# Optimization experiments

Measured on AMD Instinct MI355X. Metric: run time of the kernel, lower is better.

Reference implementation:

```python
import jax, jax.numpy as jnp
import numpy as np

B, C, H, W = 8, 256, 32, 32
N_HEAD = 4
EPS = 1e-5


def setup_inputs() -> dict:
    key = jax.random.key(0)
    ks = jax.random.split(key, 8)
    return {
        "input": jax.random.normal(ks[0], (B, C, H, W), dtype=jnp.float32),
        "bn_gamma": jnp.ones((C,), dtype=jnp.float32),
        "bn_beta": jnp.zeros((C,), dtype=jnp.float32),
        "bn_mean": jax.random.normal(ks[1], (C,), dtype=jnp.float32) * 0.1,
        "bn_var": jax.random.uniform(ks[2], (C,), dtype=jnp.float32, minval=0.5, maxval=1.5),
        "dw_w": jax.random.normal(ks[3], (C,), dtype=jnp.float32) * (1.0 / np.sqrt(C)),
        "pw_w": jax.random.normal(ks[4], (3 * C, C), dtype=jnp.float32) * (1.0 / np.sqrt(C)),
        "out_w": jax.random.normal(ks[5], (C, C), dtype=jnp.float32) * (1.0 / np.sqrt(C)),
        "out_b": jnp.zeros((C,), dtype=jnp.float32),
    }


def reference(input, bn_gamma, bn_beta, bn_mean, bn_var, dw_w, pw_w, out_w, out_b):
    b, c, h, w = input.shape
    n_head = N_HEAD
    head_dim = c // n_head

    # BatchNorm2d (eval mode: running stats), fused with depthwise 1x1 conv
    # (groups=C, kernel 1x1 -> per-channel scalar multiply).
    scale = (bn_gamma * jax.lax.rsqrt(bn_var + EPS) * dw_w)[None, :, None, None]
    shift = (bn_beta * dw_w)[None, :, None, None]
    mean = bn_mean[None, :, None, None]
    x = (input - mean) * scale + shift  # [B,C,H,W]

    # Pointwise 1x1 conv -> QKV: [B, 3C, H, W]
    qkv = jnp.einsum('oc,bchw->bohw', pw_w, x)
    qkv = qkv.reshape(b, n_head, head_dim * 3, h, w)
    q, k, v = jnp.split(qkv, 3, axis=2)  # each [B,n,d,H,W]

    # Full spatial attention logits: [B, n, H, W, H, W]
    attn = jnp.einsum('bnchw,bncyx->bnhwyx', q, k) * (1.0 / np.sqrt(head_dim))
    # Faithful to original: softmax over LAST axis (key x/width) ONLY.
    attn = jax.nn.softmax(attn, axis=-1)

    out = jnp.einsum('bnhwyx,bncyx->bnchw', attn, v).reshape(b, c, h, w)
    out = jnp.einsum('oc,bchw->bohw', out_w, out) + out_b[None, :, None, None]
    return out + input
```

## Files before the change

kernel.cpp:

```cpp
#include <hip/hip_runtime.h>

#define NB 8
#define NC 256
#define NS 1024
#define NHEAD 4
#define HD 64
#define OC 768

#define QSCALE 0.1803368801111204f

typedef float f32x4 __attribute__((ext_vector_type(4)));
typedef __bf16 bf16x8 __attribute__((ext_vector_type(8)));
typedef unsigned short u16;
typedef unsigned int u32;
typedef u16 u16x8 __attribute__((ext_vector_type(8)));
typedef u32 u32x2 __attribute__((ext_vector_type(2)));
typedef int i32x4 __attribute__((ext_vector_type(4)));

__device__ __forceinline__ u16 f2b(float f) {
    return __builtin_bit_cast(u16, (__bf16)f);
}
__device__ __forceinline__ u32 pack2(float lo, float hi) {
    return (u32)f2b(lo) | ((u32)f2b(hi) << 16);
}

__device__ __forceinline__ f32x4 MFMA(u16x8 a, u16x8 b, f32x4 c) {
    return __builtin_amdgcn_mfma_f32_16x16x32_bf16(
        __builtin_bit_cast(bf16x8, a), __builtin_bit_cast(bf16x8, b), c, 0, 0, 0);
}

__global__ void xform(const float* __restrict__ in,
                      const float* __restrict__ gma, const float* __restrict__ bta,
                      const float* __restrict__ mu,  const float* __restrict__ var,
                      const float* __restrict__ dw,  u16* __restrict__ xt) {
    __shared__ float tile[32][33];
    __shared__ float ssc[32], ssh[32];
    int b = blockIdx.z, c0 = blockIdx.y * 32, s0 = blockIdx.x * 32;
    int tx = threadIdx.x & 31, ty = threadIdx.x >> 5;
    if (threadIdx.x < 32) {
        int c = c0 + threadIdx.x;
        float sc = gma[c] * rsqrtf(var[c] + 1e-5f) * dw[c];
        ssc[threadIdx.x] = sc;
        ssh[threadIdx.x] = bta[c] * dw[c] - mu[c] * sc;
    }
    __syncthreads();
#pragma unroll
    for (int r = 0; r < 4; r++) {
        int c = ty + r * 8;
        tile[c][tx] = in[((size_t)b * NC + c0 + c) * NS + s0 + tx] * ssc[c] + ssh[c];
    }
    __syncthreads();
#pragma unroll
    for (int r = 0; r < 4; r++) {
        int s = ty + r * 8;
        xt[((size_t)b * NS + s0 + s) * NC + c0 + tx] = f2b(tile[tx][s]);
    }
}

__global__ __launch_bounds__(256) void qkv_gemm(const float* __restrict__ pw, const u16* __restrict__ xt,
                                                u16* __restrict__ qb, u16* __restrict__ kb,
                                                u16* __restrict__ vb) {
    __shared__ __attribute__((aligned(16))) u16 Ws[64][72];
    __shared__ __attribute__((aligned(16))) u16 Xs[128][72];
    int b = blockIdx.z;
    int m0 = blockIdx.y * 64, n0 = blockIdx.x * 128;
    int tid = threadIdx.x, lane = tid & 63, w = tid >> 6, lg = lane >> 4, li = lane & 15;
    int rowA = tid >> 2, colA = (tid & 3) * 16;
    int rowB = tid >> 1, colB = (tid & 1) * 32;
    const float* pA = pw + (size_t)(m0 + rowA) * NC + colA;
    const u16*   pB = xt + ((size_t)b * NS + n0 + rowB) * NC + colB;
    f32x4 acc[4][2] = {};
#pragma unroll
    for (int k0 = 0; k0 < NC; k0 += 64) {
        __syncthreads();
        f32x4 a0 = *(const f32x4*)(pA + k0);
        f32x4 a1 = *(const f32x4*)(pA + k0 + 4);
        f32x4 a2 = *(const f32x4*)(pA + k0 + 8);
        f32x4 a3 = *(const f32x4*)(pA + k0 + 12);
        i32x4 tb0 = *(const i32x4*)(pB + k0);
        i32x4 tb1 = *(const i32x4*)(pB + k0 + 8);
        i32x4 tb2 = *(const i32x4*)(pB + k0 + 16);
        i32x4 tb3 = *(const i32x4*)(pB + k0 + 24);
        i32x4 wa0, wa1;
        wa0[0] = pack2(a0[0], a0[1]); wa0[1] = pack2(a0[2], a0[3]);
        wa0[2] = pack2(a1[0], a1[1]); wa0[3] = pack2(a1[2], a1[3]);
        wa1[0] = pack2(a2[0], a2[1]); wa1[1] = pack2(a2[2], a2[3]);
        wa1[2] = pack2(a3[0], a3[1]); wa1[3] = pack2(a3[2], a3[3]);
        *(i32x4*)&Ws[rowA][colA]     = wa0;
        *(i32x4*)&Ws[rowA][colA + 8] = wa1;
        *(i32x4*)&Xs[rowB][colB]      = tb0;
        *(i32x4*)&Xs[rowB][colB + 8]  = tb1;
        *(i32x4*)&Xs[rowB][colB + 16] = tb2;
        *(i32x4*)&Xs[rowB][colB + 24] = tb3;
        __syncthreads();
        u16x8 af[4][2], bfr[2][2];
#pragma unroll
        for (int mf = 0; mf < 4; mf++)
#pragma unroll
            for (int kc = 0; kc < 2; kc++)
                af[mf][kc] = *(const u16x8*)&Ws[mf * 16 + li][kc * 32 + lg * 8];
#pragma unroll
        for (int nf = 0; nf < 2; nf++)
#pragma unroll
            for (int kc = 0; kc < 2; kc++)
                bfr[nf][kc] = *(const u16x8*)&Xs[w * 32 + nf * 16 + li][kc * 32 + lg * 8];
#pragma unroll
        for (int kc = 0; kc < 2; kc++)
#pragma unroll
            for (int mf = 0; mf < 4; mf++)
#pragma unroll
                for (int nf = 0; nf < 2; nf++)
                    acc[mf][nf] = MFMA(af[mf][kc], bfr[nf][kc], acc[mf][nf]);
    }
    int sel = (m0 >> 6) % 3;
    int n = m0 / 192;
    size_t bn = (size_t)b * NHEAD + n;
    if (sel == 0) {
#pragma unroll
        for (int mf = 0; mf < 4; mf++)
#pragma unroll
            for (int nf = 0; nf < 2; nf++) {
                int d0 = mf * 16 + lg * 4;
                int s = n0 + w * 32 + nf * 16 + li;
                u32x2 pk;
                pk[0] = pack2(acc[mf][nf][0] * QSCALE, acc[mf][nf][1] * QSCALE);
                pk[1] = pack2(acc[mf][nf][2] * QSCALE, acc[mf][nf][3] * QSCALE);
                *(u32x2*)(qb + (bn * NS + s) * HD + d0) = pk;
            }
    } else if (sel == 1) {
#pragma unroll
        for (int mf = 0; mf < 4; mf++)
#pragma unroll
            for (int nf = 0; nf < 2; nf++) {
                int d0 = mf * 16 + lg * 4;
                int s = n0 + w * 32 + nf * 16 + li;
                u32x2 pk;
                pk[0] = pack2(acc[mf][nf][0], acc[mf][nf][1]);
                pk[1] = pack2(acc[mf][nf][2], acc[mf][nf][3]);
                *(u32x2*)(kb + (bn * NS + s) * HD + d0) = pk;
            }
    } else {
#pragma unroll
        for (int mf = 0; mf < 4; mf++)
#pragma unroll
            for (int j = 0; j < 4; j++) {
                int r = mf * 16 + lg * 4 + j;
#pragma unroll
                for (int nf = 0; nf < 2; nf++) {
                    int s = n0 + w * 32 + nf * 16 + li;
                    vb[(bn * HD + r) * NS + s] = f2b(acc[mf][nf][j]);
                }
            }
    }
}

#define SMEM_K 0
#define SMEM_V 9216
#define SMEM_P 18432
#define SMEM_BYTES 38912
__global__ __launch_bounds__(256) void attn_k(const u16* __restrict__ qbuf, const u16* __restrict__ kbuf,
                                              const u16* __restrict__ vbuf, u16* __restrict__ ao0,
                                              u16* __restrict__ ao1) {
    __shared__ __attribute__((aligned(16))) char smem[SMEM_BYTES];
    u16 (*Ks)[72] = (u16(*)[72])(smem + SMEM_K);
    u16 (*Vs)[72] = (u16(*)[72])(smem + SMEM_V);
    u16 (*Ps)[64][40] = (u16(*)[64][40])(smem + SMEM_P);
    float (*red)[68] = (float(*)[68])smem;
    int b = blockIdx.z, n = blockIdx.y;
    int s0 = (blockIdx.x >> 1) * 128;
    int th = blockIdx.x & 1;
    u16* aoh = th ? ao1 : ao0;
    size_t bn = (size_t)b * NHEAD + n;
    const u16* qg = qbuf + (bn * NS + s0) * HD;
    const u16* kg = kbuf + (bn * NS + th * 512) * HD;
    const u16* vg = vbuf + bn * HD * NS + th * 512;
    int tid = threadIdx.x, lane = tid & 63, w = tid >> 6, lg = lane >> 4, li = lane & 15;
    int tq = w & 1, tt = w >> 1;
    int srow = tid >> 2, sc8 = (tid & 3) * 16;
    i32x4 rk0 = *(const i32x4*)(kg + srow * HD + sc8);
    i32x4 rk1 = *(const i32x4*)(kg + srow * HD + sc8 + 8);
    i32x4 rv0 = *(const i32x4*)(vg + srow * NS + sc8);
    i32x4 rv1 = *(const i32x4*)(vg + srow * NS + sc8 + 8);
    u16x8 bq[4][2];
#pragma unroll
    for (int qf = 0; qf < 4; qf++)
#pragma unroll
        for (int kc = 0; kc < 2; kc++)
            bq[qf][kc] = *(const u16x8*)(qg + (tq * 64 + qf * 16 + li) * HD + kc * 32 + lg * 8);
    f32x4 oacc[4][4] = {};
    for (int t0 = 0; t0 < 512; t0 += 64) {
        __syncthreads();
        *(i32x4*)&Ks[srow][sc8]     = rk0;
        *(i32x4*)&Ks[srow][sc8 + 8] = rk1;
        *(i32x4*)&Vs[srow][sc8]     = rv0;
        *(i32x4*)&Vs[srow][sc8 + 8] = rv1;
        __syncthreads();
        if (t0 + 64 < 512) {
            rk0 = *(const i32x4*)(kg + (t0 + 64 + srow) * HD + sc8);
            rk1 = *(const i32x4*)(kg + (t0 + 64 + srow) * HD + sc8 + 8);
            rv0 = *(const i32x4*)(vg + srow * NS + t0 + 64 + sc8);
            rv1 = *(const i32x4*)(vg + srow * NS + t0 + 64 + sc8 + 8);
        }
        u16x8 ak[2][2];
#pragma unroll
        for (int tf = 0; tf < 2; tf++)
#pragma unroll
            for (int kc = 0; kc < 2; kc++)
                ak[tf][kc] = *(const u16x8*)&Ks[tt * 32 + tf * 16 + li][kc * 32 + lg * 8];
        f32x4 sacc[2][4];
        __builtin_amdgcn_s_setprio(1);
#pragma unroll
        for (int tf = 0; tf < 2; tf++)
#pragma unroll
            for (int qf = 0; qf < 4; qf++) {
                f32x4 z = {0.f, 0.f, 0.f, 0.f};
                z = MFMA(ak[tf][0], bq[qf][0], z);
                sacc[tf][qf] = MFMA(ak[tf][1], bq[qf][1], z);
            }
        __builtin_amdgcn_s_setprio(0);
        u32x2 pp[4][2];
#pragma unroll
        for (int qf = 0; qf < 4; qf++) {
            float p[8];
            float sum = 0.f;
#pragma unroll
            for (int j = 0; j < 4; j++) { p[j] = exp2f(sacc[0][qf][j]); sum += p[j]; }
#pragma unroll
            for (int j = 0; j < 4; j++) { p[4 + j] = exp2f(sacc[1][qf][j]); sum += p[4 + j]; }
            sum += __shfl_xor(sum, 16);
            sum += __shfl_xor(sum, 32);
            float inv = 1.0f / sum;
#pragma unroll
            for (int tf = 0; tf < 2; tf++) {
                u32x2 pk;
                pk[0] = pack2(p[tf * 4 + 0] * inv, p[tf * 4 + 1] * inv);
                pk[1] = pack2(p[tf * 4 + 2] * inv, p[tf * 4 + 3] * inv);
                pp[qf][tf] = pk;
            }
        }
#pragma unroll
        for (int qf = 0; qf < 4; qf++)
#pragma unroll
            for (int tf = 0; tf < 2; tf++)
                *(u32x2*)&Ps[w][qf * 16 + li][tf * 16 + lg * 4] = pp[qf][tf];
        u16x8 pa[4];
#pragma unroll
        for (int qf = 0; qf < 4; qf++)
            pa[qf] = *(const u16x8*)&Ps[w][qf * 16 + li][lg * 8];
        u16x8 bv[4];
#pragma unroll
        for (int nf = 0; nf < 4; nf++)
            bv[nf] = *(const u16x8*)&Vs[nf * 16 + li][tt * 32 + lg * 8];
        __builtin_amdgcn_s_setprio(1);
#pragma unroll
        for (int qf = 0; qf < 4; qf++)
#pragma unroll
            for (int nf = 0; nf < 4; nf++)
                oacc[qf][nf] = MFMA(pa[qf], bv[nf], oacc[qf][nf]);
        __builtin_amdgcn_s_setprio(0);
    }
    __syncthreads();
    if (tt == 1) {
#pragma unroll
        for (int qf = 0; qf < 4; qf++)
#pragma unroll
            for (int nf = 0; nf < 4; nf++)
#pragma unroll
                for (int j = 0; j < 4; j++)
                    red[tq * 64 + qf * 16 + lg * 4 + j][nf * 16 + li] = oacc[qf][nf][j];
    }
    __syncthreads();
    if (tt == 0) {
#pragma unroll
        for (int qf = 0; qf < 4; qf++)
#pragma unroll
            for (int nf = 0; nf < 4; nf++)
#pragma unroll
                for (int j = 0; j < 4; j++) {
                    int s = s0 + tq * 64 + qf * 16 + lg * 4 + j;
                    int c = n * HD + nf * 16 + li;
                    float v = oacc[qf][nf][j] + red[tq * 64 + qf * 16 + lg * 4 + j][nf * 16 + li];
                    aoh[((size_t)b * NS + s) * NC + c] = f2b(v);
                }
    }
}

__global__ __launch_bounds__(256) void out_gemm(const float* __restrict__ ow, const u16* __restrict__ ao0,
                                                const u16* __restrict__ ao1,
                                                const float* __restrict__ outb, const float* __restrict__ in,
                                                float* __restrict__ out) {
    __shared__ __attribute__((aligned(16))) u16 Ws[64][72];
    __shared__ __attribute__((aligned(16))) u16 Xs[128][72];
    int b = blockIdx.z;
    int m0 = blockIdx.y * 64, n0 = blockIdx.x * 128;
    int tid = threadIdx.x, lane = tid & 63, w = tid >> 6, lg = lane >> 4, li = lane & 15;
    int rowA = tid >> 2, colA = (tid & 3) * 16;
    int rowB = tid >> 1, colB = (tid & 1) * 32;
    const float* pA = ow + (size_t)(m0 + rowA) * NC + colA;
    size_t boff = ((size_t)b * NS + n0 + rowB) * NC + colB;
    f32x4 acc[4][2] = {};
#pragma unroll
    for (int k0 = 0; k0 < 2 * NC; k0 += 64) {
        const u16* pB = (k0 < NC ? ao0 : ao1) + boff + (k0 & (NC - 1));
        int ka = k0 & (NC - 1);
        __syncthreads();
        f32x4 a0 = *(const f32x4*)(pA + ka);
        f32x4 a1 = *(const f32x4*)(pA + ka + 4);
        f32x4 a2 = *(const f32x4*)(pA + ka + 8);
        f32x4 a3 = *(const f32x4*)(pA + ka + 12);
        i32x4 tb0 = *(const i32x4*)(pB);
        i32x4 tb1 = *(const i32x4*)(pB + 8);
        i32x4 tb2 = *(const i32x4*)(pB + 16);
        i32x4 tb3 = *(const i32x4*)(pB + 24);
        i32x4 wa0, wa1;
        wa0[0] = pack2(a0[0], a0[1]); wa0[1] = pack2(a0[2], a0[3]);
        wa0[2] = pack2(a1[0], a1[1]); wa0[3] = pack2(a1[2], a1[3]);
        wa1[0] = pack2(a2[0], a2[1]); wa1[1] = pack2(a2[2], a2[3]);
        wa1[2] = pack2(a3[0], a3[1]); wa1[3] = pack2(a3[2], a3[3]);
        *(i32x4*)&Ws[rowA][colA]     = wa0;
        *(i32x4*)&Ws[rowA][colA + 8] = wa1;
        *(i32x4*)&Xs[rowB][colB]      = tb0;
        *(i32x4*)&Xs[rowB][colB + 8]  = tb1;
        *(i32x4*)&Xs[rowB][colB + 16] = tb2;
        *(i32x4*)&Xs[rowB][colB + 24] = tb3;
        __syncthreads();
        u16x8 af[4][2], bfr[2][2];
#pragma unroll
        for (int mf = 0; mf < 4; mf++)
#pragma unroll
            for (int kc = 0; kc < 2; kc++)
                af[mf][kc] = *(const u16x8*)&Ws[mf * 16 + li][kc * 32 + lg * 8];
#pragma unroll
        for (int nf = 0; nf < 2; nf++)
#pragma unroll
            for (int kc = 0; kc < 2; kc++)
                bfr[nf][kc] = *(const u16x8*)&Xs[w * 32 + nf * 16 + li][kc * 32 + lg * 8];
#pragma unroll
        for (int kc = 0; kc < 2; kc++)
#pragma unroll
            for (int mf = 0; mf < 4; mf++)
#pragma unroll
                for (int nf = 0; nf < 2; nf++)
                    acc[mf][nf] = MFMA(af[mf][kc], bfr[nf][kc], acc[mf][nf]);
    }
#pragma unroll
    for (int mf = 0; mf < 4; mf++)
#pragma unroll
        for (int j = 0; j < 4; j++) {
            int o = m0 + mf * 16 + lg * 4 + j;
            float bias = outb[o];
#pragma unroll
            for (int nf = 0; nf < 2; nf++) {
                int s = n0 + w * 32 + nf * 16 + li;
                size_t idx = ((size_t)b * NC + o) * NS + s;
                out[idx] = acc[mf][nf][j] + bias + in[idx];
            }
        }
}

extern "C" void kernel_launch(void* const* d_in, const int* in_sizes, int n_in,
                              void* d_out, int out_size, void* d_ws, size_t ws_size,
                              hipStream_t stream) {
    const float* input = (const float*)d_in[0];
    const float* gma = (const float*)d_in[1];
    const float* bta = (const float*)d_in[2];
    const float* mu  = (const float*)d_in[3];
    const float* var = (const float*)d_in[4];
    const float* dw  = (const float*)d_in[5];
    const float* pw  = (const float*)d_in[6];
    const float* ow  = (const float*)d_in[7];
    const float* ob  = (const float*)d_in[8];
    float* out = (float*)d_out;
    char* ws = (char*)d_ws;

    const size_t SZ_BIG = (size_t)NB * NS * NC * 2;
    u16* xt  = (u16*)(ws);
    u16* qb  = (u16*)(ws + SZ_BIG);
    u16* kb  = (u16*)(ws + 2 * SZ_BIG);
    u16* vb  = (u16*)(ws + 3 * SZ_BIG);
    u16* ao1 = (u16*)(ws + 4 * SZ_BIG);
    u16* ao0 = xt;

    xform<<<dim3(32, 8, 8), 256, 0, stream>>>(input, gma, bta, mu, var, dw, xt);
    qkv_gemm<<<dim3(8, 12, 8), 256, 0, stream>>>(pw, xt, qb, kb, vb);
    attn_k<<<dim3(16, 4, 8), 256, 0, stream>>>(qb, kb, vb, ao0, ao1);
    out_gemm<<<dim3(8, 4, 8), 256, 0, stream>>>(ow, ao0, ao1, ob, input, out);
}
```

Before: 59.94 us.

## Fuse BatchNorm transform and transpose into QKV GEMM operand loading

Removes the separate xform kernel that normalized the input and wrote a transposed bf16 copy. The QKV GEMM now reads the fp32 input directly, applies the per-channel scale and shift from a shared-memory table, converts to bf16 and transposes into the LDS tile. This saves one launch and a write plus read of an intermediate buffer. In exchange, each of the 12 M-tile blocks re-reads and re-converts the fp32 input, so global read traffic doubles in width and is repeated. The LDS stores are scattered 4-byte writes that may cause bank conflicts.

```diff
diff --git a/kernel.cpp b/kernel.cpp
--- a/kernel.cpp
+++ b/kernel.cpp
@@ -29,58 +29,45 @@
         __builtin_bit_cast(bf16x8, a), __builtin_bit_cast(bf16x8, b), c, 0, 0, 0);
 }
 
-__global__ void xform(const float* __restrict__ in,
-                      const float* __restrict__ gma, const float* __restrict__ bta,
-                      const float* __restrict__ mu,  const float* __restrict__ var,
-                      const float* __restrict__ dw,  u16* __restrict__ xt) {
-    __shared__ float tile[32][33];
-    __shared__ float ssc[32], ssh[32];
-    int b = blockIdx.z, c0 = blockIdx.y * 32, s0 = blockIdx.x * 32;
-    int tx = threadIdx.x & 31, ty = threadIdx.x >> 5;
-    if (threadIdx.x < 32) {
-        int c = c0 + threadIdx.x;
-        float sc = gma[c] * rsqrtf(var[c] + 1e-5f) * dw[c];
-        ssc[threadIdx.x] = sc;
-        ssh[threadIdx.x] = bta[c] * dw[c] - mu[c] * sc;
-    }
-    __syncthreads();
-#pragma unroll
-    for (int r = 0; r < 4; r++) {
-        int c = ty + r * 8;
-        tile[c][tx] = in[((size_t)b * NC + c0 + c) * NS + s0 + tx] * ssc[c] + ssh[c];
-    }
-    __syncthreads();
-#pragma unroll
-    for (int r = 0; r < 4; r++) {
-        int s = ty + r * 8;
-        xt[((size_t)b * NS + s0 + s) * NC + c0 + tx] = f2b(tile[tx][s]);
-    }
-}
-
-__global__ __launch_bounds__(256) void qkv_gemm(const float* __restrict__ pw, const u16* __restrict__ xt,
+__global__ __launch_bounds__(256) void qkv_gemm(const float* __restrict__ in,
+                                                const float* __restrict__ gma, const float* __restrict__ bta,
+                                                const float* __restrict__ mu,  const float* __restrict__ var,
+                                                const float* __restrict__ dw,  const float* __restrict__ pw,
                                                 u16* __restrict__ qb, u16* __restrict__ kb,
                                                 u16* __restrict__ vb) {
     __shared__ __attribute__((aligned(16))) u16 Ws[64][72];
     __shared__ __attribute__((aligned(16))) u16 Xs[128][72];
+    __shared__ __attribute__((aligned(16))) float ssb[NC][2];
     int b = blockIdx.z;
     int m0 = blockIdx.y * 64, n0 = blockIdx.x * 128;
     int tid = threadIdx.x, lane = tid & 63, w = tid >> 6, lg = lane >> 4, li = lane & 15;
     int rowA = tid >> 2, colA = (tid & 3) * 16;
-    int rowB = tid >> 1, colB = (tid & 1) * 32;
+    int c2l = (tid & 31) * 2, sg = tid >> 5;
+    {
+        float sc = gma[tid] * rsqrtf(var[tid] + 1e-5f) * dw[tid];
+        ssb[tid][0] = sc;
+        ssb[tid][1] = bta[tid] * dw[tid] - mu[tid] * sc;
+    }
     const float* pA = pw + (size_t)(m0 + rowA) * NC + colA;
-    const u16*   pB = xt + ((size_t)b * NS + n0 + rowB) * NC + colB;
+    const float* pX = in + (size_t)b * NC * NS + n0 + sg * 16;
+    __syncthreads();
     f32x4 acc[4][2] = {};
 #pragma unroll
     for (int k0 = 0; k0 < NC; k0 += 64) {
-        __syncthreads();
         f32x4 a0 = *(const f32x4*)(pA + k0);
         f32x4 a1 = *(const f32x4*)(pA + k0 + 4);
         f32x4 a2 = *(const f32x4*)(pA + k0 + 8);
         f32x4 a3 = *(const f32x4*)(pA + k0 + 12);
-        i32x4 tb0 = *(const i32x4*)(pB + k0);
-        i32x4 tb1 = *(const i32x4*)(pB + k0 + 8);
-        i32x4 tb2 = *(const i32x4*)(pB + k0 + 16);
-        i32x4 tb3 = *(const i32x4*)(pB + k0 + 24);
+        int c2 = k0 + c2l;
+        const float* px0 = pX + (size_t)c2 * NS;
+        f32x4 xa[4], xb[4];
+#pragma unroll
+        for (int i = 0; i < 4; i++) {
+            xa[i] = *(const f32x4*)(px0 + i * 4);
+            xb[i] = *(const f32x4*)(px0 + NS + i * 4);
+        }
+        f32x4 ss = *(const f32x4*)&ssb[c2][0];
+        __syncthreads();
         i32x4 wa0, wa1;
         wa0[0] = pack2(a0[0], a0[1]); wa0[1] = pack2(a0[2], a0[3]);
         wa0[2] = pack2(a1[0], a1[1]); wa0[3] = pack2(a1[2], a1[3]);
@@ -88,10 +75,13 @@
         wa1[2] = pack2(a3[0], a3[1]); wa1[3] = pack2(a3[2], a3[3]);
         *(i32x4*)&Ws[rowA][colA]     = wa0;
         *(i32x4*)&Ws[rowA][colA + 8] = wa1;
-        *(i32x4*)&Xs[rowB][colB]      = tb0;
-        *(i32x4*)&Xs[rowB][colB + 8]  = tb1;
-        *(i32x4*)&Xs[rowB][colB + 16] = tb2;
-        *(i32x4*)&Xs[rowB][colB + 24] = tb3;
+#pragma unroll
+        for (int i = 0; i < 4; i++)
+#pragma unroll
+            for (int j = 0; j < 4; j++) {
+                u32 v = pack2(xa[i][j] * ss[0] + ss[1], xb[i][j] * ss[2] + ss[3]);
+                *(u32*)&Xs[sg * 16 + i * 4 + j][c2l] = v;
+            }
         __syncthreads();
         u16x8 af[4][2], bfr[2][2];
 #pragma unroll
@@ -374,15 +364,13 @@
     char* ws = (char*)d_ws;
 
     const size_t SZ_BIG = (size_t)NB * NS * NC * 2;
-    u16* xt  = (u16*)(ws);
-    u16* qb  = (u16*)(ws + SZ_BIG);
-    u16* kb  = (u16*)(ws + 2 * SZ_BIG);
-    u16* vb  = (u16*)(ws + 3 * SZ_BIG);
+    u16* qb  = (u16*)(ws);
+    u16* kb  = (u16*)(ws + SZ_BIG);
+    u16* vb  = (u16*)(ws + 2 * SZ_BIG);
+    u16* ao0 = (u16*)(ws + 3 * SZ_BIG);
     u16* ao1 = (u16*)(ws + 4 * SZ_BIG);
-    u16* ao0 = xt;
-
-    xform<<<dim3(32, 8, 8), 256, 0, stream>>>(input, gma, bta, mu, var, dw, xt);
-    qkv_gemm<<<dim3(8, 12, 8), 256, 0, stream>>>(pw, xt, qb, kb, vb);
+
+    qkv_gemm<<<dim3(8, 12, 8), 256, 0, stream>>>(input, gma, bta, mu, var, dw, pw, qb, kb, vb);
     attn_k<<<dim3(16, 4, 8), 256, 0, stream>>>(qb, kb, vb, ao0, ao1);
     out_gemm<<<dim3(8, 4, 8), 256, 0, stream>>>(ow, ao0, ao1, ob, input, out);
 }
```

Result: slower. 63.06 us (+5.2%).

## Feed softmax probabilities directly to 16x16x16 MFMA, skip LDS round trip

Applied to the files above, without the earlier changes.

In the attention kernel, the bf16 probability fragments now feed 16x16x16 bf16 MFMAs straight from registers. The accumulator layout matches the A-operand layout, so the write to shared memory and the read back for the PV product go away. That also shrinks LDS use, at the cost of twice as many smaller MFMA instructions and narrower V loads. Separately, both GEMM kernels now issue their global loads before the barrier so load latency overlaps with waiting for other waves.

```diff
diff --git a/kernel.cpp b/kernel.cpp
--- a/kernel.cpp
+++ b/kernel.cpp
@@ -16,6 +16,7 @@
 typedef u16 u16x8 __attribute__((ext_vector_type(8)));
 typedef u32 u32x2 __attribute__((ext_vector_type(2)));
 typedef int i32x4 __attribute__((ext_vector_type(4)));
+typedef short s16x4 __attribute__((ext_vector_type(4)));
 
 __device__ __forceinline__ u16 f2b(float f) {
     return __builtin_bit_cast(u16, (__bf16)f);
@@ -72,7 +73,6 @@
     f32x4 acc[4][2] = {};
 #pragma unroll
     for (int k0 = 0; k0 < NC; k0 += 64) {
-        __syncthreads();
         f32x4 a0 = *(const f32x4*)(pA + k0);
         f32x4 a1 = *(const f32x4*)(pA + k0 + 4);
         f32x4 a2 = *(const f32x4*)(pA + k0 + 8);
@@ -81,6 +81,7 @@
         i32x4 tb1 = *(const i32x4*)(pB + k0 + 8);
         i32x4 tb2 = *(const i32x4*)(pB + k0 + 16);
         i32x4 tb3 = *(const i32x4*)(pB + k0 + 24);
+        __syncthreads();
         i32x4 wa0, wa1;
         wa0[0] = pack2(a0[0], a0[1]); wa0[1] = pack2(a0[2], a0[3]);
         wa0[2] = pack2(a1[0], a1[1]); wa0[3] = pack2(a1[2], a1[3]);
@@ -156,15 +157,23 @@
 
 #define SMEM_K 0
 #define SMEM_V 9216
+#if __has_builtin(__builtin_amdgcn_mfma_f32_16x16x16bf16_1k)
+#define PV16 1
+#define SMEM_BYTES 34816
+#else
+#define PV16 0
 #define SMEM_P 18432
 #define SMEM_BYTES 38912
+#endif
 __global__ __launch_bounds__(256) void attn_k(const u16* __restrict__ qbuf, const u16* __restrict__ kbuf,
                                               const u16* __restrict__ vbuf, u16* __restrict__ ao0,
                                               u16* __restrict__ ao1) {
     __shared__ __attribute__((aligned(16))) char smem[SMEM_BYTES];
     u16 (*Ks)[72] = (u16(*)[72])(smem + SMEM_K);
     u16 (*Vs)[72] = (u16(*)[72])(smem + SMEM_V);
+#if !PV16
     u16 (*Ps)[64][40] = (u16(*)[64][40])(smem + SMEM_P);
+#endif
     float (*red)[68] = (float(*)[68])smem;
     int b = blockIdx.z, n = blockIdx.y;
     int s0 = (blockIdx.x >> 1) * 128;
@@ -238,6 +247,26 @@
                 pp[qf][tf] = pk;
             }
         }
+#if PV16
+        s16x4 bv16[4][2];
+#pragma unroll
+        for (int nf = 0; nf < 4; nf++)
+#pragma unroll
+            for (int tf = 0; tf < 2; tf++)
+                bv16[nf][tf] = *(const s16x4*)&Vs[nf * 16 + li][tt * 32 + tf * 16 + lg * 4];
+        __builtin_amdgcn_s_setprio(1);
+#pragma unroll
+        for (int qf = 0; qf < 4; qf++) {
+            s16x4 pa0 = __builtin_bit_cast(s16x4, pp[qf][0]);
+            s16x4 pa1 = __builtin_bit_cast(s16x4, pp[qf][1]);
+#pragma unroll
+            for (int nf = 0; nf < 4; nf++) {
+                oacc[qf][nf] = __builtin_amdgcn_mfma_f32_16x16x16bf16_1k(pa0, bv16[nf][0], oacc[qf][nf], 0, 0, 0);
+                oacc[qf][nf] = __builtin_amdgcn_mfma_f32_16x16x16bf16_1k(pa1, bv16[nf][1], oacc[qf][nf], 0, 0, 0);
+            }
+        }
+        __builtin_amdgcn_s_setprio(0);
+#else
 #pragma unroll
         for (int qf = 0; qf < 4; qf++)
 #pragma unroll
@@ -258,6 +287,7 @@
             for (int nf = 0; nf < 4; nf++)
                 oacc[qf][nf] = MFMA(pa[qf], bv[nf], oacc[qf][nf]);
         __builtin_amdgcn_s_setprio(0);
+#endif
     }
     __syncthreads();
     if (tt == 1) {
@@ -303,7 +333,6 @@
     for (int k0 = 0; k0 < 2 * NC; k0 += 64) {
         const u16* pB = (k0 < NC ? ao0 : ao1) + boff + (k0 & (NC - 1));
         int ka = k0 & (NC - 1);
-        __syncthreads();
         f32x4 a0 = *(const f32x4*)(pA + ka);
         f32x4 a1 = *(const f32x4*)(pA + ka + 4);
         f32x4 a2 = *(const f32x4*)(pA + ka + 8);
@@ -312,6 +341,7 @@
         i32x4 tb1 = *(const i32x4*)(pB + 8);
         i32x4 tb2 = *(const i32x4*)(pB + 16);
         i32x4 tb3 = *(const i32x4*)(pB + 24);
+        __syncthreads();
         i32x4 wa0, wa1;
         wa0[0] = pack2(a0[0], a0[1]); wa0[1] = pack2(a0[2], a0[3]);
         wa0[2] = pack2(a1[0], a1[1]); wa0[3] = pack2(a1[2], a1[3]);
```

Result: faster. 58.73 us (-2.0%).
